# Optimization experiments

Hardware: AMD Instinct MI355X
Metric: run time of the kernel (lower is better)

## Reference

```python
import jax, jax.numpy as jnp
import numpy as np

EMBED_DIM = 1024
MEMORY_SIZE = 64
TOPK = 3
LN_EPS = 1e-5


def setup_inputs() -> dict:
    key = jax.random.key(0)
    ks = jax.random.split(key, 8)
    D, M = EMBED_DIM, MEMORY_SIZE
    scale = 1.0 / np.sqrt(D)
    x = jax.random.normal(ks[0], (8, 2048, D), dtype=jnp.float32)
    memory = jax.random.normal(ks[1], (M, D), dtype=jnp.float32) * scale
    Wq = jax.random.normal(ks[2], (D, D), dtype=jnp.float32) * scale
    bq = jnp.zeros((D,), dtype=jnp.float32)
    Wf = jax.random.normal(ks[3], (D, 2 * D), dtype=jnp.float32) * (1.0 / np.sqrt(2 * D))
    bf = jnp.zeros((D,), dtype=jnp.float32)
    gamma = jnp.ones((D,), dtype=jnp.float32)
    beta = jnp.zeros((D,), dtype=jnp.float32)
    return {"x": x, "memory": memory, "Wq": Wq, "bq": bq,
            "Wf": Wf, "bf": bf, "gamma": gamma, "beta": beta}


def reference(x, memory, Wq, bq, Wf, bf, gamma, beta):
    B, S, D = x.shape
    # query projection: [B,S,D]
    query = jnp.einsum('bsd,ed->bse', x, Wq) + bq
    # similarity to memory bank: [B,S,M]
    sim = jnp.einsum('bsd,md->bsm', query, memory)
    # top-k over memory slots
    topk_sim, topk_idx = jax.lax.top_k(sim, TOPK)            # [B,S,K]
    weights = jax.nn.softmax(topk_sim, axis=-1)               # [B,S,K]
    retrieved = memory[topk_idx]                              # [B,S,K,D]
    memory_output = jnp.einsum('bskd,bsk->bsd', retrieved, weights)
    # fusion MLP: Linear(2D->D) -> LayerNorm -> ReLU
    cat = jnp.concatenate([x, memory_output], axis=-1)        # [B,S,2D]
    h = jnp.einsum('bsc,dc->bsd', cat, Wf) + bf
    mean = jnp.mean(h, axis=-1, keepdims=True)
    var = jnp.mean(jnp.square(h - mean), axis=-1, keepdims=True)
    h = (h - mean) * jax.lax.rsqrt(var + LN_EPS) * gamma + beta
    return jax.nn.relu(h)
```

## Files before the change

kernel.cpp:

```cpp
#include <hip/hip_runtime.h>

#define DCH 1024
#define MSLOT 64
#define NTOK 16384

typedef __bf16 bf16x8 __attribute__((ext_vector_type(8)));
typedef float f32x4 __attribute__((ext_vector_type(4)));
typedef unsigned short u16x8 __attribute__((ext_vector_type(8)));
typedef unsigned short u16x4 __attribute__((ext_vector_type(4)));

__device__ __forceinline__ unsigned short f2bf(float f) {
  unsigned u = __float_as_uint(f);
  u += 0x7fffu + ((u >> 16) & 1u);
  return (unsigned short)(u >> 16);
}
__device__ __forceinline__ float bf2f(unsigned short s) {
  return __uint_as_float(((unsigned)s) << 16);
}

__device__ __forceinline__ void gld16(const void* g, void* l) {
  __builtin_amdgcn_global_load_lds((const __attribute__((address_space(1))) void*)g,
                                   (__attribute__((address_space(3))) void*)l, 16, 0, 0);
}

__global__ __launch_bounds__(256) void prep_a_kernel(
    const float* __restrict__ Wf, float* __restrict__ Wf2T,
    unsigned short* __restrict__ Wf1b,
    const float* __restrict__ bq, const float* __restrict__ memv,
    float* __restrict__ sc) {
  __shared__ float tile[64][65];
  __shared__ float red[256];
  const int b = blockIdx.x, tid = threadIdx.x;

  if (b >= 257) {
    const int j = b - 257;
#pragma unroll
    for (int i = 0; i < 16; ++i) {
      int f4 = j * 4096 + i * 256 + tid;
      int row = f4 >> 8, c4 = (f4 & 255) * 4;
      float4 v = *(const float4*)(Wf + (size_t)row * 2048 + c4);
      u16x4 o = {f2bf(v.x), f2bf(v.y), f2bf(v.z), f2bf(v.w)};
      *(u16x4*)(Wf1b + row * 1024 + c4) = o;
    }
  } else if (b >= 1) {
    const int t = b - 1;
    const int c0 = (t & 15) * 64, d0 = (t >> 4) * 64;
    const int lane = tid & 63, wv = tid >> 6;
#pragma unroll
    for (int i = 0; i < 16; ++i) {
      int r = wv + i * 4;
      tile[r][lane] = Wf[(size_t)(d0 + r) * 2048 + 1024 + c0 + lane];
    }
    __syncthreads();
#pragma unroll
    for (int i = 0; i < 16; ++i) {
      int r = wv + i * 4;
      Wf2T[(size_t)(c0 + r) * 1024 + d0 + lane] = tile[lane][r];
    }
  } else {
    int m = tid >> 2, q = tid & 3;
    float s = 0.f;
    for (int e = q * 256; e < q * 256 + 256; ++e) s += bq[e] * memv[m * 1024 + e];
    red[tid] = s;
    __syncthreads();
    if (tid < 64) sc[tid] = red[tid * 4] + red[tid * 4 + 1] + red[tid * 4 + 2] + red[tid * 4 + 3];
  }
}

__global__ __launch_bounds__(256) void prep_b_kernel(
    const float* __restrict__ memv, const float* __restrict__ Wq,
    const float* __restrict__ Wf2T,
    float* __restrict__ partWm, float* __restrict__ partP) {
  int b = blockIdx.x;
  const int tid = threadIdx.x;
  const int which = b >> 7;
  b &= 127;
  const int kc = b & 7, dt = (b >> 3) & 3, mg = b >> 5;
  const float* B = which ? Wf2T : Wq;
  float* outp = which ? partP : partWm;
  const int d = dt * 256 + tid;
  const int e0 = kc * 128;
  const int m0 = mg * 16;

  float acc[16];
#pragma unroll
  for (int m = 0; m < 16; ++m) acc[m] = 0.f;

  const float* bp = B + (size_t)e0 * 1024 + d;
  const float* mp = memv + m0 * 1024 + e0;
#pragma unroll 4
  for (int e = 0; e < 128; ++e) {
    float wv = bp[(size_t)e * 1024];
#pragma unroll
    for (int m = 0; m < 16; ++m) acc[m] += mp[m * 1024 + e] * wv;
  }
  float* op = outp + ((size_t)kc * 64 + m0) * 1024 + d;
#pragma unroll
  for (int m = 0; m < 16; ++m) op[m * 1024] = acc[m];
}

__global__ __launch_bounds__(256) void prep_c_kernel(
    const float* __restrict__ partWm, const float* __restrict__ partP,
    unsigned short* __restrict__ Wmb, float* __restrict__ P) {
  int idx = blockIdx.x * 256 + threadIdx.x;
  if (idx < 65536) {
    float s = 0.f;
#pragma unroll
    for (int k = 0; k < 8; ++k) s += partWm[k * 65536 + idx];
    Wmb[idx] = f2bf(s);
  } else {
    idx -= 65536;
    float s = 0.f;
#pragma unroll
    for (int k = 0; k < 8; ++k) s += partP[k * 65536 + idx];
    P[idx] = s;
  }
}

__global__ __launch_bounds__(256) void sim_topk_kernel(
    const float* __restrict__ x, unsigned short* __restrict__ xb,
    const unsigned short* __restrict__ Wmb,
    const float* __restrict__ sc, float4* __restrict__ meta) {
  __shared__ __attribute__((aligned(16))) unsigned short As[64 * 64];
  __shared__ __attribute__((aligned(16))) unsigned short Bs[64 * 64];
  __shared__ float sim_s[64 * 65];
  const int tid = threadIdx.x;
  const int wave = tid >> 6, lane = tid & 63;
  const int tok0 = blockIdx.x * 64;
  const int quad = lane >> 4, cl = lane & 15;
  const int sw = ((lane & 7) ^ (lane >> 3)) * 8;
  const int cx0 = ((quad) ^ (cl & 7)) * 8;
  const int cx1 = ((quad + 4) ^ (cl & 7)) * 8;

  f32x4 acc[4];
#pragma unroll
  for (int j = 0; j < 4; ++j) acc[j] = {0.f, 0.f, 0.f, 0.f};

  for (int kt = 0; kt < 16; ++kt) {
    __syncthreads();
#pragma unroll
    for (int i = 0; i < 2; ++i) {
      int ch = (wave * 2 + i) * 64 + lane;
      int row = ch >> 3;
      const float* xp = x + (size_t)(tok0 + row) * 1024 + kt * 64 + sw;
      float4 v0 = *(const float4*)(xp);
      float4 v1 = *(const float4*)(xp + 4);
      u16x8 o = {f2bf(v0.x), f2bf(v0.y), f2bf(v0.z), f2bf(v0.w),
                 f2bf(v1.x), f2bf(v1.y), f2bf(v1.z), f2bf(v1.w)};
      *(u16x8*)(As + ch * 8) = o;
      *(u16x8*)(xb + (size_t)(tok0 + row) * 1024 + kt * 64 + sw) = o;
      gld16(Wmb + row * 1024 + kt * 64 + sw, Bs + ch * 8);
    }
    __syncthreads();
#pragma unroll
    for (int ks = 0; ks < 2; ++ks) {
      const int cx = ks ? cx1 : cx0;
      bf16x8 a = *(const bf16x8*)(As + (wave * 16 + cl) * 64 + cx);
#pragma unroll
      for (int nt = 0; nt < 4; ++nt) {
        bf16x8 bb = *(const bf16x8*)(Bs + (cl + nt * 16) * 64 + cx);
        acc[nt] = __builtin_amdgcn_mfma_f32_16x16x32_bf16(a, bb, acc[nt], 0, 0, 0);
      }
    }
  }
#pragma unroll
  for (int nt = 0; nt < 4; ++nt)
#pragma unroll
    for (int r = 0; r < 4; ++r) {
      int lt = wave * 16 + quad * 4 + r;
      int mc = nt * 16 + cl;
      sim_s[lt * 65 + mc] = acc[nt][r] + sc[mc];
    }
  __syncthreads();
  if (tid < 64) {
    const float* sp = sim_s + tid * 65;
    float s0 = -1e30f, s1 = -1e30f, s2 = -1e30f;
    int i0 = 0, i1 = 0, i2 = 0;
    for (int m = 0; m < 64; ++m) {
      float v = sp[m];
      if (v > s0) { s2 = s1; i2 = i1; s1 = s0; i1 = i0; s0 = v; i0 = m; }
      else if (v > s1) { s2 = s1; i2 = i1; s1 = v; i1 = m; }
      else if (v > s2) { s2 = v; i2 = m; }
    }
    float e1 = __expf(s1 - s0), e2 = __expf(s2 - s0);
    float inv = 1.f / (1.f + e1 + e2);
    meta[tok0 + tid] = make_float4(inv, e1 * inv, e2 * inv,
                                   __int_as_float(i0 | (i1 << 8) | (i2 << 16)));
  }
}

__global__ __launch_bounds__(256, 2) void gemm_h_kernel(
    const unsigned short* __restrict__ xb, const unsigned short* __restrict__ Wf1b,
    unsigned short* __restrict__ hb) {
  __shared__ __attribute__((aligned(16))) unsigned short As[256 * 64];
  __shared__ __attribute__((aligned(16))) unsigned short Bs[128 * 64];
  const int tid = threadIdx.x;
  const int wave = tid >> 6, lane = tid & 63;
  const int b = blockIdx.x;
  const int tok0 = (b & 63) * 256, d0 = (b >> 6) * 128;
  const int quad = lane >> 4, cl = lane & 15;
  const int wm = wave * 64;
  const int sw = ((lane & 7) ^ (lane >> 3)) * 8;
  const int cx0 = ((quad) ^ (cl & 7)) * 8;
  const int cx1 = ((quad + 4) ^ (cl & 7)) * 8;

  f32x4 acc[4][8];
#pragma unroll
  for (int i = 0; i < 4; ++i)
#pragma unroll
    for (int j = 0; j < 8; ++j) acc[i][j] = {0.f, 0.f, 0.f, 0.f};

  for (int kt = 0; kt < 16; ++kt) {
    __syncthreads();
#pragma unroll
    for (int i = 0; i < 8; ++i) {
      int ch = (wave * 8 + i) * 64 + lane;
      int row = ch >> 3;
      gld16(xb + (size_t)(tok0 + row) * 1024 + kt * 64 + sw, As + ch * 8);
    }
#pragma unroll
    for (int i = 0; i < 4; ++i) {
      int ch = (wave * 4 + i) * 64 + lane;
      int row = ch >> 3;
      gld16(Wf1b + (size_t)(d0 + row) * 1024 + kt * 64 + sw, Bs + ch * 8);
    }
    __syncthreads();
#pragma unroll
    for (int ks = 0; ks < 2; ++ks) {
      const int cx = ks ? cx1 : cx0;
      bf16x8 a[4], bb[8];
#pragma unroll
      for (int t = 0; t < 4; ++t)
        a[t] = *(const bf16x8*)(As + (wm + cl + t * 16) * 64 + cx);
#pragma unroll
      for (int t = 0; t < 8; ++t)
        bb[t] = *(const bf16x8*)(Bs + (cl + t * 16) * 64 + cx);
#pragma unroll
      for (int mt = 0; mt < 4; ++mt)
#pragma unroll
        for (int nt = 0; nt < 8; ++nt)
          acc[mt][nt] = __builtin_amdgcn_mfma_f32_16x16x32_bf16(a[mt], bb[nt], acc[mt][nt], 0, 0, 0);
    }
  }

#pragma unroll
  for (int mt = 0; mt < 4; ++mt) {
#pragma unroll
    for (int r = 0; r < 4; ++r) {
      int row = tok0 + wm + mt * 16 + quad * 4 + r;
#pragma unroll
      for (int nt = 0; nt < 8; ++nt) {
        int d = d0 + nt * 16 + cl;
        hb[(size_t)row * 1024 + d] = f2bf(acc[mt][nt][r]);
      }
    }
  }
}

__global__ __launch_bounds__(256) void ln_relu_kernel(
    const unsigned short* __restrict__ hb, const float* __restrict__ P,
    const float4* __restrict__ meta, const float* __restrict__ bfv,
    const float* __restrict__ gamma, const float* __restrict__ beta,
    float* __restrict__ out) {
  const int tid = threadIdx.x;
  const int wave = tid >> 6, lane = tid & 63;
  const int t = blockIdx.x * 4 + wave;

  float4 mv = meta[t];
  int pk = __float_as_int(mv.w);
  const float* P0 = P + (pk & 255) * 1024;
  const float* P1 = P + ((pk >> 8) & 255) * 1024;
  const float* P2 = P + ((pk >> 16) & 255) * 1024;

  const unsigned short* hp = hb + (size_t)t * 1024;

  u16x4 hv[4];
  float4 b4[4], p0[4], p1[4], p2[4];
#pragma unroll
  for (int j = 0; j < 4; ++j) {
    const int off = (j * 64 + lane) * 4;
    hv[j] = *(const u16x4*)(hp + off);
    b4[j] = *(const float4*)(bfv + off);
    p0[j] = *(const float4*)(P0 + off);
    p1[j] = *(const float4*)(P1 + off);
    p2[j] = *(const float4*)(P2 + off);
  }

  float f[16];
#pragma unroll
  for (int j = 0; j < 4; ++j) {
    f[j * 4 + 0] = bf2f(hv[j][0]) + b4[j].x + mv.x * p0[j].x + mv.y * p1[j].x + mv.z * p2[j].x;
    f[j * 4 + 1] = bf2f(hv[j][1]) + b4[j].y + mv.x * p0[j].y + mv.y * p1[j].y + mv.z * p2[j].y;
    f[j * 4 + 2] = bf2f(hv[j][2]) + b4[j].z + mv.x * p0[j].z + mv.y * p1[j].z + mv.z * p2[j].z;
    f[j * 4 + 3] = bf2f(hv[j][3]) + b4[j].w + mv.x * p0[j].w + mv.y * p1[j].w + mv.z * p2[j].w;
  }
  float s = 0.f, q = 0.f;
#pragma unroll
  for (int j = 0; j < 16; ++j) { s += f[j]; q += f[j] * f[j]; }
#pragma unroll
  for (int off = 32; off; off >>= 1) {
    s += __shfl_xor(s, off);
    q += __shfl_xor(q, off);
  }
  float mean = s * (1.f / 1024.f);
  float var = q * (1.f / 1024.f) - mean * mean;
  float rs = rsqrtf(var + 1e-5f);
  float* op = out + (size_t)t * 1024;
#pragma unroll
  for (int j = 0; j < 4; ++j) {
    const int off = (j * 64 + lane) * 4;
    float4 g4 = *(const float4*)(gamma + off);
    float4 e4 = *(const float4*)(beta + off);
    float4 v;
    v.x = fmaxf((f[j * 4 + 0] - mean) * rs * g4.x + e4.x, 0.f);
    v.y = fmaxf((f[j * 4 + 1] - mean) * rs * g4.y + e4.y, 0.f);
    v.z = fmaxf((f[j * 4 + 2] - mean) * rs * g4.z + e4.z, 0.f);
    v.w = fmaxf((f[j * 4 + 3] - mean) * rs * g4.w + e4.w, 0.f);
    *(float4*)(op + off) = v;
  }
}

extern "C" void kernel_launch(void* const* d_in, const int* in_sizes, int n_in,
                              void* d_out, int out_size, void* d_ws, size_t ws_size,
                              hipStream_t stream) {
  const float* x     = (const float*)d_in[0];
  const float* memv  = (const float*)d_in[1];
  const float* Wq    = (const float*)d_in[2];
  const float* bq    = (const float*)d_in[3];
  const float* Wf    = (const float*)d_in[4];
  const float* bfv   = (const float*)d_in[5];
  const float* gamma = (const float*)d_in[6];
  const float* beta  = (const float*)d_in[7];
  float* out = (float*)d_out;
  char* ws = (char*)d_ws;

  unsigned short* Wf1b   = (unsigned short*)(ws);
  unsigned short* Wmb    = (unsigned short*)(ws + 2097152);
  float*          P      = (float*)(ws + 2228224);
  float*          sc     = (float*)(ws + 2490368);
  float4*         meta   = (float4*)(ws + 2490624);
  float*          Wf2T   = (float*)(ws + 2752768);
  float*          partWm = (float*)(ws + 6947072);
  float*          partP  = (float*)(ws + 9044224);
  unsigned short* xb     = (unsigned short*)(ws + 11141376);
  unsigned short* hb     = (unsigned short*)(ws + 44695808);

  hipLaunchKernelGGL(prep_a_kernel, dim3(321), dim3(256), 0, stream,
                     Wf, Wf2T, Wf1b, bq, memv, sc);
  hipLaunchKernelGGL(prep_b_kernel, dim3(256), dim3(256), 0, stream,
                     memv, Wq, Wf2T, partWm, partP);
  hipLaunchKernelGGL(prep_c_kernel, dim3(512), dim3(256), 0, stream,
                     partWm, partP, Wmb, P);
  hipLaunchKernelGGL(sim_topk_kernel, dim3(256), dim3(256), 0, stream,
                     x, xb, Wmb, sc, meta);
  hipLaunchKernelGGL(gemm_h_kernel, dim3(512), dim3(256), 0, stream,
                     xb, Wf1b, hb);
  hipLaunchKernelGGL(ln_relu_kernel, dim3(4096), dim3(256), 0, stream,
                     hb, P, meta, bfv, gamma, beta, out);
}
```

Baseline: 238.2 us.

## Split similarity GEMM over K into partial sums with separate top-k reduction kernel

The fused similarity+top-k kernel, which launched only 256 blocks, is split into a K-split partial GEMM over 1024 blocks that writes fp32 partial similarity tiles to workspace. A new top-k kernel sums the four partials, adds the bias term and runs the top-3 selection and softmax. The aim is to fill more of the GPU's compute units during the x-to-bf16 conversion and similarity pass. The cost is an extra launch and a partial-sum buffer that reuses the hb workspace region, which is safe only because gemm_h writes hb afterwards.

```diff
diff --git a/kernel.cpp b/kernel.cpp
--- a/kernel.cpp
+++ b/kernel.cpp
@@ -117,16 +117,15 @@
   }
 }
 
-__global__ __launch_bounds__(256) void sim_topk_kernel(
+__global__ __launch_bounds__(256) void sim_part_kernel(
     const float* __restrict__ x, unsigned short* __restrict__ xb,
-    const unsigned short* __restrict__ Wmb,
-    const float* __restrict__ sc, float4* __restrict__ meta) {
+    const unsigned short* __restrict__ Wmb, float* __restrict__ psim) {
   __shared__ __attribute__((aligned(16))) unsigned short As[64 * 64];
   __shared__ __attribute__((aligned(16))) unsigned short Bs[64 * 64];
-  __shared__ float sim_s[64 * 65];
   const int tid = threadIdx.x;
   const int wave = tid >> 6, lane = tid & 63;
-  const int tok0 = blockIdx.x * 64;
+  const int tile = blockIdx.x & 255, ks = blockIdx.x >> 8;
+  const int tok0 = tile * 64;
   const int quad = lane >> 4, cl = lane & 15;
   const int sw = ((lane & 7) ^ (lane >> 3)) * 8;
   const int cx0 = ((quad) ^ (cl & 7)) * 8;
@@ -136,7 +135,8 @@
 #pragma unroll
   for (int j = 0; j < 4; ++j) acc[j] = {0.f, 0.f, 0.f, 0.f};
 
-  for (int kt = 0; kt < 16; ++kt) {
+  for (int kt4 = 0; kt4 < 4; ++kt4) {
+    const int kt = ks * 4 + kt4;
     __syncthreads();
 #pragma unroll
     for (int i = 0; i < 2; ++i) {
@@ -153,8 +153,8 @@
     }
     __syncthreads();
 #pragma unroll
-    for (int ks = 0; ks < 2; ++ks) {
-      const int cx = ks ? cx1 : cx0;
+    for (int kss = 0; kss < 2; ++kss) {
+      const int cx = kss ? cx1 : cx0;
       bf16x8 a = *(const bf16x8*)(As + (wave * 16 + cl) * 64 + cx);
 #pragma unroll
       for (int nt = 0; nt < 4; ++nt) {
@@ -163,29 +163,64 @@
       }
     }
   }
+  float* pp = psim + (size_t)(ks * 256 + tile) * 4096;
 #pragma unroll
   for (int nt = 0; nt < 4; ++nt)
 #pragma unroll
     for (int r = 0; r < 4; ++r) {
       int lt = wave * 16 + quad * 4 + r;
       int mc = nt * 16 + cl;
-      sim_s[lt * 65 + mc] = acc[nt][r] + sc[mc];
-    }
+      pp[lt * 64 + mc] = acc[nt][r];
+    }
+}
+
+__global__ __launch_bounds__(256) void topk_kernel(
+    const float* __restrict__ psim, const float* __restrict__ sc,
+    float4* __restrict__ meta) {
+  __shared__ float sim_s[64 * 65];
+  const int tid = threadIdx.x;
+  const int tile = blockIdx.x;
+  const int tok = tid >> 2, mb = (tid & 3) * 16;
+
+  const float* p = psim + (size_t)tile * 4096 + tok * 64 + mb;
+  float v[16];
+#pragma unroll
+  for (int j4 = 0; j4 < 4; ++j4) {
+    float4 a = *(const float4*)(p + j4 * 4);
+    v[j4 * 4 + 0] = a.x; v[j4 * 4 + 1] = a.y; v[j4 * 4 + 2] = a.z; v[j4 * 4 + 3] = a.w;
+  }
+#pragma unroll
+  for (int k = 1; k < 4; ++k) {
+    const float* q = p + (size_t)k * 256 * 4096;
+#pragma unroll
+    for (int j4 = 0; j4 < 4; ++j4) {
+      float4 a = *(const float4*)(q + j4 * 4);
+      v[j4 * 4 + 0] += a.x; v[j4 * 4 + 1] += a.y; v[j4 * 4 + 2] += a.z; v[j4 * 4 + 3] += a.w;
+    }
+  }
+#pragma unroll
+  for (int j4 = 0; j4 < 4; ++j4) {
+    float4 s4 = *(const float4*)(sc + mb + j4 * 4);
+    sim_s[tok * 65 + mb + j4 * 4 + 0] = v[j4 * 4 + 0] + s4.x;
+    sim_s[tok * 65 + mb + j4 * 4 + 1] = v[j4 * 4 + 1] + s4.y;
+    sim_s[tok * 65 + mb + j4 * 4 + 2] = v[j4 * 4 + 2] + s4.z;
+    sim_s[tok * 65 + mb + j4 * 4 + 3] = v[j4 * 4 + 3] + s4.w;
+  }
   __syncthreads();
   if (tid < 64) {
     const float* sp = sim_s + tid * 65;
     float s0 = -1e30f, s1 = -1e30f, s2 = -1e30f;
     int i0 = 0, i1 = 0, i2 = 0;
     for (int m = 0; m < 64; ++m) {
-      float v = sp[m];
-      if (v > s0) { s2 = s1; i2 = i1; s1 = s0; i1 = i0; s0 = v; i0 = m; }
-      else if (v > s1) { s2 = s1; i2 = i1; s1 = v; i1 = m; }
-      else if (v > s2) { s2 = v; i2 = m; }
+      float vv = sp[m];
+      if (vv > s0) { s2 = s1; i2 = i1; s1 = s0; i1 = i0; s0 = vv; i0 = m; }
+      else if (vv > s1) { s2 = s1; i2 = i1; s1 = vv; i1 = m; }
+      else if (vv > s2) { s2 = vv; i2 = m; }
     }
     float e1 = __expf(s1 - s0), e2 = __expf(s2 - s0);
     float inv = 1.f / (1.f + e1 + e2);
-    meta[tok0 + tid] = make_float4(inv, e1 * inv, e2 * inv,
-                                   __int_as_float(i0 | (i1 << 8) | (i2 << 16)));
+    meta[tile * 64 + tid] = make_float4(inv, e1 * inv, e2 * inv,
+                                        __int_as_float(i0 | (i1 << 8) | (i2 << 16)));
   }
 }
 
@@ -344,6 +379,7 @@
   float*          partP  = (float*)(ws + 9044224);
   unsigned short* xb     = (unsigned short*)(ws + 11141376);
   unsigned short* hb     = (unsigned short*)(ws + 44695808);
+  float*          psim   = (float*)(ws + 44695808);
 
   hipLaunchKernelGGL(prep_a_kernel, dim3(321), dim3(256), 0, stream,
                      Wf, Wf2T, Wf1b, bq, memv, sc);
@@ -351,8 +387,10 @@
                      memv, Wq, Wf2T, partWm, partP);
   hipLaunchKernelGGL(prep_c_kernel, dim3(512), dim3(256), 0, stream,
                      partWm, partP, Wmb, P);
-  hipLaunchKernelGGL(sim_topk_kernel, dim3(256), dim3(256), 0, stream,
-                     x, xb, Wmb, sc, meta);
+  hipLaunchKernelGGL(sim_part_kernel, dim3(1024), dim3(256), 0, stream,
+                     x, xb, Wmb, psim);
+  hipLaunchKernelGGL(topk_kernel, dim3(256), dim3(256), 0, stream,
+                     psim, sc, meta);
   hipLaunchKernelGGL(gemm_h_kernel, dim3(512), dim3(256), 0, stream,
                      xb, Wf1b, hb);
   hipLaunchKernelGGL(ln_relu_kernel, dim3(4096), dim3(256), 0, stream,
```

Result: no change. 242.7 us (+1.9%).

## Shrink sim_topk tile to 16 tokens per block and launch four times more blocks

Applied to the files above, without the earlier changes.

The similarity/top-k kernel now processes 16 tokens per block instead of 64, with each wave computing a different 16-slot column slice of the memory bank rather than its own 16 tokens. The grid grows from 256 to 1024 blocks so the 256-CU GPU gets more blocks and better latency hiding on the streaming read of x. The cost is that the Wmb tile is reloaded four times as often, only half the threads load x, and only 16 threads do the top-k scan.

```diff
diff --git a/kernel.cpp b/kernel.cpp
--- a/kernel.cpp
+++ b/kernel.cpp
@@ -121,20 +121,21 @@
     const float* __restrict__ x, unsigned short* __restrict__ xb,
     const unsigned short* __restrict__ Wmb,
     const float* __restrict__ sc, float4* __restrict__ meta) {
-  __shared__ __attribute__((aligned(16))) unsigned short As[64 * 64];
+  __shared__ __attribute__((aligned(16))) unsigned short As[16 * 64];
   __shared__ __attribute__((aligned(16))) unsigned short Bs[64 * 64];
-  __shared__ float sim_s[64 * 65];
+  __shared__ float sim_s[16 * 65];
   const int tid = threadIdx.x;
   const int wave = tid >> 6, lane = tid & 63;
-  const int tok0 = blockIdx.x * 64;
+  const int tok0 = blockIdx.x * 16;
   const int quad = lane >> 4, cl = lane & 15;
   const int sw = ((lane & 7) ^ (lane >> 3)) * 8;
   const int cx0 = ((quad) ^ (cl & 7)) * 8;
   const int cx1 = ((quad + 4) ^ (cl & 7)) * 8;
 
-  f32x4 acc[4];
-#pragma unroll
-  for (int j = 0; j < 4; ++j) acc[j] = {0.f, 0.f, 0.f, 0.f};
+  const int arow = tid >> 3, acc_ = tid & 7;
+  const int alc = acc_ ^ (arow & 7);
+
+  f32x4 acc = {0.f, 0.f, 0.f, 0.f};
 
   for (int kt = 0; kt < 16; ++kt) {
     __syncthreads();
@@ -142,37 +143,34 @@
     for (int i = 0; i < 2; ++i) {
       int ch = (wave * 2 + i) * 64 + lane;
       int row = ch >> 3;
-      const float* xp = x + (size_t)(tok0 + row) * 1024 + kt * 64 + sw;
-      float4 v0 = *(const float4*)(xp);
-      float4 v1 = *(const float4*)(xp + 4);
+      gld16(Wmb + row * 1024 + kt * 64 + sw, Bs + ch * 8);
+    }
+    if (tid < 128) {
+      const size_t goff = (size_t)(tok0 + arow) * 1024 + kt * 64 + alc * 8;
+      float4 v0 = *(const float4*)(x + goff);
+      float4 v1 = *(const float4*)(x + goff + 4);
       u16x8 o = {f2bf(v0.x), f2bf(v0.y), f2bf(v0.z), f2bf(v0.w),
                  f2bf(v1.x), f2bf(v1.y), f2bf(v1.z), f2bf(v1.w)};
-      *(u16x8*)(As + ch * 8) = o;
-      *(u16x8*)(xb + (size_t)(tok0 + row) * 1024 + kt * 64 + sw) = o;
-      gld16(Wmb + row * 1024 + kt * 64 + sw, Bs + ch * 8);
+      *(u16x8*)(As + tid * 8) = o;
+      *(u16x8*)(xb + goff) = o;
     }
     __syncthreads();
 #pragma unroll
     for (int ks = 0; ks < 2; ++ks) {
       const int cx = ks ? cx1 : cx0;
-      bf16x8 a = *(const bf16x8*)(As + (wave * 16 + cl) * 64 + cx);
-#pragma unroll
-      for (int nt = 0; nt < 4; ++nt) {
-        bf16x8 bb = *(const bf16x8*)(Bs + (cl + nt * 16) * 64 + cx);
-        acc[nt] = __builtin_amdgcn_mfma_f32_16x16x32_bf16(a, bb, acc[nt], 0, 0, 0);
-      }
-    }
-  }
-#pragma unroll
-  for (int nt = 0; nt < 4; ++nt)
-#pragma unroll
-    for (int r = 0; r < 4; ++r) {
-      int lt = wave * 16 + quad * 4 + r;
-      int mc = nt * 16 + cl;
-      sim_s[lt * 65 + mc] = acc[nt][r] + sc[mc];
-    }
+      bf16x8 a = *(const bf16x8*)(As + cl * 64 + cx);
+      bf16x8 bb = *(const bf16x8*)(Bs + (wave * 16 + cl) * 64 + cx);
+      acc = __builtin_amdgcn_mfma_f32_16x16x32_bf16(a, bb, acc, 0, 0, 0);
+    }
+  }
+#pragma unroll
+  for (int r = 0; r < 4; ++r) {
+    int lt = quad * 4 + r;
+    int mc = wave * 16 + cl;
+    sim_s[lt * 65 + mc] = acc[r] + sc[mc];
+  }
   __syncthreads();
-  if (tid < 64) {
+  if (tid < 16) {
     const float* sp = sim_s + tid * 65;
     float s0 = -1e30f, s1 = -1e30f, s2 = -1e30f;
     int i0 = 0, i1 = 0, i2 = 0;
@@ -351,7 +349,7 @@
                      memv, Wq, Wf2T, partWm, partP);
   hipLaunchKernelGGL(prep_c_kernel, dim3(512), dim3(256), 0, stream,
                      partWm, partP, Wmb, P);
-  hipLaunchKernelGGL(sim_topk_kernel, dim3(256), dim3(256), 0, stream,
+  hipLaunchKernelGGL(sim_topk_kernel, dim3(1024), dim3(256), 0, stream,
                      x, xb, Wmb, sc, meta);
   hipLaunchKernelGGL(gemm_h_kernel, dim3(512), dim3(256), 0, stream,
                      xb, Wf1b, hb);
```

After: 241.2 us. About the same (+1.2%).
